# Kernel tuning notes

Measured on AMD Instinct MI355X. Metric: run time of the kernel, lower is better.

## Reference

```python
import jax, jax.numpy as jnp
import numpy as np

N, OBS_LEN, PRED_LEN = 8192, 20, 30
EMBED, HIDDEN, CNN_OUT = 64, 128, 2048


def setup_inputs() -> dict:
    key = jax.random.key(0)
    ks = jax.random.split(key, 13)
    s = 0.05
    return {
        "img_embedding": jax.random.normal(ks[0], (N, CNN_OUT), jnp.float32),
        "obs_pos": jax.random.normal(ks[1], (N, OBS_LEN, 2), jnp.float32),
        "obs_hist_size": jax.random.randint(ks[2], (N,), 0, 20, jnp.int64) if jax.config.jax_enable_x64 else jax.random.randint(ks[2], (N,), 0, 20, jnp.int32),
        "obs_pos_rel": jax.random.normal(ks[3], (N, OBS_LEN, 2), jnp.float32),
        "h0": jax.random.normal(ks[4], (1, HIDDEN), jnp.float32) * s,
        "W_ih": jax.random.normal(ks[5], (4 * HIDDEN, EMBED), jnp.float32) * s,
        "W_hh": jax.random.normal(ks[6], (4 * HIDDEN, HIDDEN), jnp.float32) * s,
        "b_ih": jax.random.normal(ks[7], (4 * HIDDEN,), jnp.float32) * s,
        "b_hh": jax.random.normal(ks[8], (4 * HIDDEN,), jnp.float32) * s,
        "embed_W": jax.random.normal(ks[9], (EMBED, 2), jnp.float32) * s,
        "embed_b": jax.random.normal(ks[10], (EMBED,), jnp.float32) * s,
        "pred_W": jax.random.normal(ks[11], (2, HIDDEN + CNN_OUT), jnp.float32) * s,
        "pred_b": jax.random.normal(ks[12], (2,), jnp.float32) * s,
    }


def reference(img_embedding, obs_pos, obs_hist_size, obs_pos_rel,
              h0, W_ih, W_hh, b_ih, b_hh, embed_W, embed_b, pred_W, pred_b):
    n, obs_len = obs_pos.shape[0], obs_pos.shape[1]

    def lstm_cell(x_emb, h, c):
        # torch gate order: i, f, g, o
        gates = x_emb @ W_ih.T + b_ih + h @ W_hh.T + b_hh  # [n, 4H]
        i, f, g, o = jnp.split(gates, 4, axis=-1)
        c2 = jax.nn.sigmoid(f) * c + jax.nn.sigmoid(i) * jnp.tanh(g)
        h2 = jax.nn.sigmoid(o) * jnp.tanh(c2)
        return h2, c2

    def embed(rel):
        return jax.nn.relu(rel @ embed_W.T + embed_b)

    # NOTE: original code initializes BOTH h and c from h0 (faithful to source).
    h = jnp.broadcast_to(h0, (n, h0.shape[1]))
    c = h

    # ---- observation phase: t = 1 .. obs_len-1, masked update ----
    def obs_step(carry, inp):
        h, c = carry
        rel_t, t = inp
        mask = (obs_hist_size > (obs_len - t))[:, None]  # [n, 1]
        h2, c2 = lstm_cell(embed(rel_t), h, c)
        h = jnp.where(mask, h2, h)
        c = jnp.where(mask, c2, c)
        return (h, c), None

    ts = jnp.arange(1, obs_len)
    rel_seq = jnp.swapaxes(obs_pos_rel[:, 1:, :], 0, 1)  # [obs_len-1, n, 2]
    (h, c), _ = jax.lax.scan(obs_step, (h, c), (rel_seq, ts))

    def pred_step(carry, _):
        h, c, pos = carry
        disp = jnp.concatenate([h, img_embedding], axis=1) @ pred_W.T + pred_b  # [n, 2]
        pos = pos + disp
        h, c = lstm_cell(embed(disp), h, c)
        return (h, c, pos), pos

    pos0 = obs_pos[:, -1, :]
    _, traj = jax.lax.scan(pred_step, (h, c, pos0), None, length=PRED_LEN)
    return jnp.swapaxes(traj, 0, 1)  # [n, pred_len, 2]
```

## Files before the change

### kernel.cpp

```cpp
#include <hip/hip_runtime.h>

#define MBLK 32

typedef __attribute__((ext_vector_type(8))) short bf16x8;
typedef __attribute__((ext_vector_type(4))) float f32x4;

__device__ __forceinline__ unsigned short f2bf(float x){
  unsigned int u = __float_as_uint(x);
  u = u + 0x7FFFu + ((u >> 16) & 1u);
  return (unsigned short)(u >> 16);
}
__device__ __forceinline__ float bf2f(unsigned short s){
  return __uint_as_float(((unsigned int)s) << 16);
}
__device__ __forceinline__ float sigm(float x){
  return __builtin_amdgcn_rcpf(1.0f + __expf(-x));
}
__device__ __forceinline__ float tanh_(float x){
  return 1.0f - 2.0f*__builtin_amdgcn_rcpf(__expf(2.0f*x) + 1.0f);
}

__global__ __launch_bounds__(512, 2) void traj_kernel(
    const float* __restrict__ img, const float* __restrict__ obs_pos,
    const int* __restrict__ hist, const float* __restrict__ rel,
    const float* __restrict__ h0, const float* __restrict__ W_ih,
    const float* __restrict__ W_hh, const float* __restrict__ b_ih,
    const float* __restrict__ b_hh, const float* __restrict__ eW,
    const float* __restrict__ eb, const float* __restrict__ pW,
    const float* __restrict__ pb, float* __restrict__ out)
{
  __shared__ unsigned short xh[2][MBLK*200];
  __shared__ float relL[MBLK*40];
  __shared__ float pwL[256];
  __shared__ float eW0[64], eW1[64], ebL[64];
  __shared__ float imgcL[MBLK*2];

  const int tid  = threadIdx.x;
  const int wv   = tid >> 6;
  const int lane = tid & 63;
  const int q    = lane >> 4;
  const int i    = lane & 15;
  const int j    = wv*16 + i;
  const int g0   = blockIdx.x * MBLK;

  for (int idx = tid; idx < MBLK*40; idx += 512) relL[idx] = rel[g0*40 + idx];
  if (tid < 256) pwL[tid] = pW[(tid >> 7)*2176 + (tid & 127)];
  if (tid < 64){ eW0[tid] = eW[tid*2]; eW1[tid] = eW[tid*2+1]; ebL[tid] = eb[tid]; }

  {
    int m = tid >> 4, i16 = tid & 15;
    const float* row = img + (size_t)(g0 + m)*2048 + i16*128;
    const float* p0  = pW + 128 + i16*128;
    const float* p1  = pW + 2176 + 128 + i16*128;
    float s0 = 0.f, s1 = 0.f;
    #pragma unroll
    for (int v = 0; v < 32; v++){
      float4 a  = ((const float4*)row)[v];
      float4 w0 = ((const float4*)p0)[v];
      float4 w1 = ((const float4*)p1)[v];
      s0 += a.x*w0.x + a.y*w0.y + a.z*w0.z + a.w*w0.w;
      s1 += a.x*w1.x + a.y*w1.y + a.z*w1.z + a.w*w1.w;
    }
    #pragma unroll
    for (int msk = 1; msk < 16; msk <<= 1){
      s0 += __shfl_xor(s0, msk);
      s1 += __shfl_xor(s1, msk);
    }
    if (i16 == 0){ imgcL[m*2] = s0; imgcL[m*2+1] = s1; }
  }

  float h0j = h0[j];
  float bias_s[4];
  #pragma unroll
  for (int nt = 0; nt < 4; nt++) bias_s[nt] = b_ih[nt*128 + j] + b_hh[nt*128 + j];

  int   hist_s[8];
  float c_s[8], h_s[8];
  #pragma unroll
  for (int mt = 0; mt < 2; mt++)
    #pragma unroll
    for (int r = 0; r < 4; r++){
      int m = mt*16 + q*4 + r;
      hist_s[mt*4+r] = hist[g0 + m];
      c_s[mt*4+r] = h0j; h_s[mt*4+r] = h0j;
      xh[0][m*200 + 64 + j] = f2bf(h0j);
    }

  bf16x8 Bf[4][6];
  #pragma unroll
  for (int nt = 0; nt < 4; nt++){
    int row = nt*128 + j;
    #pragma unroll
    for (int kt = 0; kt < 6; kt++){
      const float* src = (kt < 2) ? (W_ih + row*64  + kt*32      + q*8)
                                  : (W_hh + row*128 + (kt-2)*32  + q*8);
      float4 lo = ((const float4*)src)[0];
      float4 hi = ((const float4*)src)[1];
      bf16x8 tf;
      tf[0]=(short)f2bf(lo.x); tf[1]=(short)f2bf(lo.y); tf[2]=(short)f2bf(lo.z); tf[3]=(short)f2bf(lo.w);
      tf[4]=(short)f2bf(hi.x); tf[5]=(short)f2bf(hi.y); tf[6]=(short)f2bf(hi.z); tf[7]=(short)f2bf(hi.w);
      Bf[nt][kt] = tf;
    }
  }

  const int dm  = tid >> 4;
  const int i16 = tid & 15;
  float pos_r = 0.f;
  if (i16 < 2) pos_r = obs_pos[(size_t)(g0 + dm)*40 + 38 + i16];

  __syncthreads();

  const float imgc0 = imgcL[dm*2], imgc1 = imgcL[dm*2+1];
  const float pb0 = pb[0], pb1 = pb[1];

  {
    int e0 = i16 << 2;
    float r0 = relL[dm*40 + 2], r1 = relL[dm*40 + 3];
    float a0 = fmaxf(0.f, r0*eW0[e0+0] + r1*eW1[e0+0] + ebL[e0+0]);
    float a1 = fmaxf(0.f, r0*eW0[e0+1] + r1*eW1[e0+1] + ebL[e0+1]);
    float a2 = fmaxf(0.f, r0*eW0[e0+2] + r1*eW1[e0+2] + ebL[e0+2]);
    float a3 = fmaxf(0.f, r0*eW0[e0+3] + r1*eW1[e0+3] + ebL[e0+3]);
    unsigned int pk0 = (unsigned int)f2bf(a0) | ((unsigned int)f2bf(a1) << 16);
    unsigned int pk1 = (unsigned int)f2bf(a2) | ((unsigned int)f2bf(a3) << 16);
    *((uint2*)&xh[0][dm*200 + e0]) = make_uint2(pk0, pk1);
  }

  int b = 0;
  f32x4 acc[2][4];

  for (int step = 0; step < 49; step++){
    const bool obs = (step < 19);
    __syncthreads();

    if (!obs){
      bf16x8 hv = *((const bf16x8*)&xh[b][dm*200 + 64 + i16*8]);
      float s0 = 0.f, s1 = 0.f;
      #pragma unroll
      for (int u = 0; u < 8; u++){
        float hfv = bf2f((unsigned short)hv[u]);
        s0 += hfv * pwL[i16*8 + u];
        s1 += hfv * pwL[128 + i16*8 + u];
      }
      s0 += __shfl_xor(s0, 1); s1 += __shfl_xor(s1, 1);
      s0 += __shfl_xor(s0, 2); s1 += __shfl_xor(s1, 2);
      s0 += __shfl_xor(s0, 4); s1 += __shfl_xor(s1, 4);
      s0 += __shfl_xor(s0, 8); s1 += __shfl_xor(s1, 8);
      float d0 = s0 + imgc0 + pb0;
      float d1 = s1 + imgc1 + pb1;
      if (i16 < 2){
        pos_r += (i16 == 0) ? d0 : d1;
        out[(size_t)(g0 + dm)*60 + (size_t)(step - 19)*2 + i16] = pos_r;
      }
      int e0 = i16 << 2;
      float a0 = fmaxf(0.f, d0*eW0[e0+0] + d1*eW1[e0+0] + ebL[e0+0]);
      float a1 = fmaxf(0.f, d0*eW0[e0+1] + d1*eW1[e0+1] + ebL[e0+1]);
      float a2 = fmaxf(0.f, d0*eW0[e0+2] + d1*eW1[e0+2] + ebL[e0+2]);
      float a3 = fmaxf(0.f, d0*eW0[e0+3] + d1*eW1[e0+3] + ebL[e0+3]);
      unsigned int pk0 = (unsigned int)f2bf(a0) | ((unsigned int)f2bf(a1) << 16);
      unsigned int pk1 = (unsigned int)f2bf(a2) | ((unsigned int)f2bf(a3) << 16);
      *((uint2*)&xh[b][dm*200 + e0]) = make_uint2(pk0, pk1);
      __syncthreads();
    }

    #pragma unroll
    for (int mt = 0; mt < 2; mt++){
      bf16x8 A[6];
      int mrow = mt*16 + i;
      #pragma unroll
      for (int kt = 0; kt < 6; kt++)
        A[kt] = *((const bf16x8*)&xh[b][mrow*200 + kt*32 + q*8]);
      #pragma unroll
      for (int nt = 0; nt < 4; nt++)
        acc[mt][nt] = (f32x4){bias_s[nt], bias_s[nt], bias_s[nt], bias_s[nt]};
      #pragma unroll
      for (int kt = 0; kt < 6; kt++)
        #pragma unroll
        for (int nt = 0; nt < 4; nt++)
          acc[mt][nt] = __builtin_amdgcn_mfma_f32_16x16x32_bf16(A[kt], Bf[nt][kt], acc[mt][nt], 0, 0, 0);
    }

    if (obs && step < 18){
      int tt = step + 2;
      int e0 = i16 << 2;
      float r0 = relL[dm*40 + tt*2], r1 = relL[dm*40 + tt*2 + 1];
      float a0 = fmaxf(0.f, r0*eW0[e0+0] + r1*eW1[e0+0] + ebL[e0+0]);
      float a1 = fmaxf(0.f, r0*eW0[e0+1] + r1*eW1[e0+1] + ebL[e0+1]);
      float a2 = fmaxf(0.f, r0*eW0[e0+2] + r1*eW1[e0+2] + ebL[e0+2]);
      float a3 = fmaxf(0.f, r0*eW0[e0+3] + r1*eW1[e0+3] + ebL[e0+3]);
      unsigned int pk0 = (unsigned int)f2bf(a0) | ((unsigned int)f2bf(a1) << 16);
      unsigned int pk1 = (unsigned int)f2bf(a2) | ((unsigned int)f2bf(a3) << 16);
      *((uint2*)&xh[b^1][dm*200 + e0]) = make_uint2(pk0, pk1);
    }

    #pragma unroll
    for (int mt = 0; mt < 2; mt++)
      #pragma unroll
      for (int r = 0; r < 4; r++){
        int sl = mt*4 + r;
        float ig = acc[mt][0][r];
        float fg = acc[mt][1][r];
        float gg = acc[mt][2][r];
        float og = acc[mt][3][r];
        float c2 = sigm(fg)*c_s[sl] + sigm(ig)*tanh_(gg);
        float h2 = sigm(og)*tanh_(c2);
        if (obs){
          bool upd = hist_s[sl] > (19 - step);
          c2 = upd ? c2 : c_s[sl];
          h2 = upd ? h2 : h_s[sl];
        }
        c_s[sl] = c2; h_s[sl] = h2;
        int m = mt*16 + q*4 + r;
        xh[b^1][m*200 + 64 + j] = f2bf(h2);
      }

    b ^= 1;
  }
}

extern "C" void kernel_launch(void* const* d_in, const int* in_sizes, int n_in,
                              void* d_out, int out_size, void* d_ws, size_t ws_size,
                              hipStream_t stream){
  const float* img     = (const float*)d_in[0];
  const float* obs_pos = (const float*)d_in[1];
  const int*   hist    = (const int*)d_in[2];
  const float* rel     = (const float*)d_in[3];
  const float* h0      = (const float*)d_in[4];
  const float* W_ih    = (const float*)d_in[5];
  const float* W_hh    = (const float*)d_in[6];
  const float* b_ih    = (const float*)d_in[7];
  const float* b_hh    = (const float*)d_in[8];
  const float* eW      = (const float*)d_in[9];
  const float* eb      = (const float*)d_in[10];
  const float* pW      = (const float*)d_in[11];
  const float* pb      = (const float*)d_in[12];
  float* out = (float*)d_out;
  hipLaunchKernelGGL(traj_kernel, dim3(8192/MBLK), dim3(512), 0, stream,
                     img, obs_pos, hist, rel, h0, W_ih, W_hh, b_ih, b_hh,
                     eW, eb, pW, pb, out);
}
```

Baseline: 268.6 us.

## Split LSTM row tiles across 16 waves and stage output-gate weights in LDS

```diff
diff --git a/kernel.cpp b/kernel.cpp
--- a/kernel.cpp
+++ b/kernel.cpp
@@ -20,7 +20,7 @@
   return 1.0f - 2.0f*__builtin_amdgcn_rcpf(__expf(2.0f*x) + 1.0f);
 }
 
-__global__ __launch_bounds__(512, 2) void traj_kernel(
+__global__ __launch_bounds__(1024, 4) void traj_kernel(
     const float* __restrict__ img, const float* __restrict__ obs_pos,
     const int* __restrict__ hist, const float* __restrict__ rel,
     const float* __restrict__ h0, const float* __restrict__ W_ih,
@@ -30,6 +30,7 @@
     const float* __restrict__ pb, float* __restrict__ out)
 {
   __shared__ unsigned short xh[2][MBLK*200];
+  __shared__ unsigned short BoL[6*8*64*8];
   __shared__ float relL[MBLK*40];
   __shared__ float pwL[256];
   __shared__ float eW0[64], eW1[64], ebL[64];
@@ -40,21 +41,24 @@
   const int lane = tid & 63;
   const int q    = lane >> 4;
   const int i    = lane & 15;
-  const int j    = wv*16 + i;
+  const int w8   = wv & 7;
+  const int mtb  = (wv >> 3) << 4;
+  const int jw   = w8*16 + i;
   const int g0   = blockIdx.x * MBLK;
-
-  for (int idx = tid; idx < MBLK*40; idx += 512) relL[idx] = rel[g0*40 + idx];
+  const int dm   = tid >> 5;
+  const int i32  = tid & 31;
+
+  for (int idx = tid; idx < MBLK*40; idx += 1024) relL[idx] = rel[g0*40 + idx];
   if (tid < 256) pwL[tid] = pW[(tid >> 7)*2176 + (tid & 127)];
   if (tid < 64){ eW0[tid] = eW[tid*2]; eW1[tid] = eW[tid*2+1]; ebL[tid] = eb[tid]; }
 
   {
-    int m = tid >> 4, i16 = tid & 15;
-    const float* row = img + (size_t)(g0 + m)*2048 + i16*128;
-    const float* p0  = pW + 128 + i16*128;
-    const float* p1  = pW + 2176 + 128 + i16*128;
+    const float* row = img + (size_t)(g0 + dm)*2048 + i32*64;
+    const float* p0  = pW + 128 + i32*64;
+    const float* p1  = pW + 2176 + 128 + i32*64;
     float s0 = 0.f, s1 = 0.f;
     #pragma unroll
-    for (int v = 0; v < 32; v++){
+    for (int v = 0; v < 16; v++){
       float4 a  = ((const float4*)row)[v];
       float4 w0 = ((const float4*)p0)[v];
       float4 w1 = ((const float4*)p1)[v];
@@ -62,38 +66,37 @@
       s1 += a.x*w1.x + a.y*w1.y + a.z*w1.z + a.w*w1.w;
     }
     #pragma unroll
-    for (int msk = 1; msk < 16; msk <<= 1){
+    for (int msk = 1; msk < 32; msk <<= 1){
       s0 += __shfl_xor(s0, msk);
       s1 += __shfl_xor(s1, msk);
     }
-    if (i16 == 0){ imgcL[m*2] = s0; imgcL[m*2+1] = s1; }
-  }
-
-  float h0j = h0[j];
+    if (i32 == 0){ imgcL[dm*2] = s0; imgcL[dm*2+1] = s1; }
+  }
+
+  float h0j = h0[jw];
   float bias_s[4];
   #pragma unroll
-  for (int nt = 0; nt < 4; nt++) bias_s[nt] = b_ih[nt*128 + j] + b_hh[nt*128 + j];
-
-  int   hist_s[8];
-  float c_s[8], h_s[8];
+  for (int nt = 0; nt < 4; nt++) bias_s[nt] = b_ih[nt*128 + jw] + b_hh[nt*128 + jw];
+
+  unsigned int thrpack = 0;
+  float c_s[4], h_s[4];
   #pragma unroll
-  for (int mt = 0; mt < 2; mt++)
-    #pragma unroll
-    for (int r = 0; r < 4; r++){
-      int m = mt*16 + q*4 + r;
-      hist_s[mt*4+r] = hist[g0 + m];
-      c_s[mt*4+r] = h0j; h_s[mt*4+r] = h0j;
-      xh[0][m*200 + 64 + j] = f2bf(h0j);
-    }
-
-  bf16x8 Bf[4][6];
+  for (int r = 0; r < 4; r++){
+    int m = mtb + q*4 + r;
+    int hv = hist[g0 + m];
+    thrpack |= ((unsigned int)(20 - hv) & 255u) << (r*8);
+    c_s[r] = h0j; h_s[r] = h0j;
+    xh[0][m*200 + 64 + jw] = f2bf(h0j);
+  }
+
+  bf16x8 Bf[3][6];
   #pragma unroll
-  for (int nt = 0; nt < 4; nt++){
-    int row = nt*128 + j;
+  for (int nt = 0; nt < 3; nt++){
+    int row = nt*128 + jw;
     #pragma unroll
     for (int kt = 0; kt < 6; kt++){
-      const float* src = (kt < 2) ? (W_ih + row*64  + kt*32      + q*8)
-                                  : (W_hh + row*128 + (kt-2)*32  + q*8);
+      const float* src = (kt < 2) ? (W_ih + row*64  + kt*32     + q*8)
+                                  : (W_hh + row*128 + (kt-2)*32 + q*8);
       float4 lo = ((const float4*)src)[0];
       float4 hi = ((const float4*)src)[1];
       bf16x8 tf;
@@ -102,116 +105,112 @@
       Bf[nt][kt] = tf;
     }
   }
-
-  const int dm  = tid >> 4;
-  const int i16 = tid & 15;
+  if (wv < 8){
+    int row = 384 + jw;
+    #pragma unroll
+    for (int kt = 0; kt < 6; kt++){
+      const float* src = (kt < 2) ? (W_ih + row*64  + kt*32     + q*8)
+                                  : (W_hh + row*128 + (kt-2)*32 + q*8);
+      float4 lo = ((const float4*)src)[0];
+      float4 hi = ((const float4*)src)[1];
+      bf16x8 tf;
+      tf[0]=(short)f2bf(lo.x); tf[1]=(short)f2bf(lo.y); tf[2]=(short)f2bf(lo.z); tf[3]=(short)f2bf(lo.w);
+      tf[4]=(short)f2bf(hi.x); tf[5]=(short)f2bf(hi.y); tf[6]=(short)f2bf(hi.z); tf[7]=(short)f2bf(hi.w);
+      *((bf16x8*)&BoL[((kt*8 + w8)*64 + lane)*8]) = tf;
+    }
+  }
+
   float pos_r = 0.f;
-  if (i16 < 2) pos_r = obs_pos[(size_t)(g0 + dm)*40 + 38 + i16];
+  if (i32 < 2) pos_r = obs_pos[(size_t)(g0 + dm)*40 + 38 + i32];
 
   __syncthreads();
 
-  const float imgc0 = imgcL[dm*2], imgc1 = imgcL[dm*2+1];
-  const float pb0 = pb[0], pb1 = pb[1];
+  const float ipb0 = imgcL[dm*2]     + pb[0];
+  const float ipb1 = imgcL[dm*2 + 1] + pb[1];
 
   {
-    int e0 = i16 << 2;
+    int e2 = i32*2;
     float r0 = relL[dm*40 + 2], r1 = relL[dm*40 + 3];
-    float a0 = fmaxf(0.f, r0*eW0[e0+0] + r1*eW1[e0+0] + ebL[e0+0]);
-    float a1 = fmaxf(0.f, r0*eW0[e0+1] + r1*eW1[e0+1] + ebL[e0+1]);
-    float a2 = fmaxf(0.f, r0*eW0[e0+2] + r1*eW1[e0+2] + ebL[e0+2]);
-    float a3 = fmaxf(0.f, r0*eW0[e0+3] + r1*eW1[e0+3] + ebL[e0+3]);
-    unsigned int pk0 = (unsigned int)f2bf(a0) | ((unsigned int)f2bf(a1) << 16);
-    unsigned int pk1 = (unsigned int)f2bf(a2) | ((unsigned int)f2bf(a3) << 16);
-    *((uint2*)&xh[0][dm*200 + e0]) = make_uint2(pk0, pk1);
+    float a0 = fmaxf(0.f, r0*eW0[e2]   + r1*eW1[e2]   + ebL[e2]);
+    float a1 = fmaxf(0.f, r0*eW0[e2+1] + r1*eW1[e2+1] + ebL[e2+1]);
+    *((unsigned int*)&xh[0][dm*200 + e2]) =
+        (unsigned int)f2bf(a0) | ((unsigned int)f2bf(a1) << 16);
   }
 
   int b = 0;
-  f32x4 acc[2][4];
-
   for (int step = 0; step < 49; step++){
     const bool obs = (step < 19);
     __syncthreads();
 
     if (!obs){
-      bf16x8 hv = *((const bf16x8*)&xh[b][dm*200 + 64 + i16*8]);
+      const unsigned short* hp = &xh[b][dm*200 + 64 + i32*4];
       float s0 = 0.f, s1 = 0.f;
       #pragma unroll
-      for (int u = 0; u < 8; u++){
-        float hfv = bf2f((unsigned short)hv[u]);
-        s0 += hfv * pwL[i16*8 + u];
-        s1 += hfv * pwL[128 + i16*8 + u];
-      }
-      s0 += __shfl_xor(s0, 1); s1 += __shfl_xor(s1, 1);
-      s0 += __shfl_xor(s0, 2); s1 += __shfl_xor(s1, 2);
-      s0 += __shfl_xor(s0, 4); s1 += __shfl_xor(s1, 4);
-      s0 += __shfl_xor(s0, 8); s1 += __shfl_xor(s1, 8);
-      float d0 = s0 + imgc0 + pb0;
-      float d1 = s1 + imgc1 + pb1;
-      if (i16 < 2){
-        pos_r += (i16 == 0) ? d0 : d1;
-        out[(size_t)(g0 + dm)*60 + (size_t)(step - 19)*2 + i16] = pos_r;
-      }
-      int e0 = i16 << 2;
-      float a0 = fmaxf(0.f, d0*eW0[e0+0] + d1*eW1[e0+0] + ebL[e0+0]);
-      float a1 = fmaxf(0.f, d0*eW0[e0+1] + d1*eW1[e0+1] + ebL[e0+1]);
-      float a2 = fmaxf(0.f, d0*eW0[e0+2] + d1*eW1[e0+2] + ebL[e0+2]);
-      float a3 = fmaxf(0.f, d0*eW0[e0+3] + d1*eW1[e0+3] + ebL[e0+3]);
-      unsigned int pk0 = (unsigned int)f2bf(a0) | ((unsigned int)f2bf(a1) << 16);
-      unsigned int pk1 = (unsigned int)f2bf(a2) | ((unsigned int)f2bf(a3) << 16);
-      *((uint2*)&xh[b][dm*200 + e0]) = make_uint2(pk0, pk1);
+      for (int u = 0; u < 4; u++){
+        float hfv = bf2f(hp[u]);
+        s0 += hfv * pwL[i32*4 + u];
+        s1 += hfv * pwL[128 + i32*4 + u];
+      }
+      #pragma unroll
+      for (int msk = 1; msk < 32; msk <<= 1){
+        s0 += __shfl_xor(s0, msk);
+        s1 += __shfl_xor(s1, msk);
+      }
+      float d0 = s0 + ipb0;
+      float d1 = s1 + ipb1;
+      if (i32 < 2){
+        pos_r += (i32 == 0) ? d0 : d1;
+        out[(size_t)(g0 + dm)*60 + (size_t)(step - 19)*2 + i32] = pos_r;
+      }
+      int e2 = i32*2;
+      float a0 = fmaxf(0.f, d0*eW0[e2]   + d1*eW1[e2]   + ebL[e2]);
+      float a1 = fmaxf(0.f, d0*eW0[e2+1] + d1*eW1[e2+1] + ebL[e2+1]);
+      *((unsigned int*)&xh[b][dm*200 + e2]) =
+          (unsigned int)f2bf(a0) | ((unsigned int)f2bf(a1) << 16);
       __syncthreads();
     }
 
-    #pragma unroll
-    for (int mt = 0; mt < 2; mt++){
-      bf16x8 A[6];
-      int mrow = mt*16 + i;
-      #pragma unroll
-      for (int kt = 0; kt < 6; kt++)
-        A[kt] = *((const bf16x8*)&xh[b][mrow*200 + kt*32 + q*8]);
-      #pragma unroll
-      for (int nt = 0; nt < 4; nt++)
-        acc[mt][nt] = (f32x4){bias_s[nt], bias_s[nt], bias_s[nt], bias_s[nt]};
-      #pragma unroll
-      for (int kt = 0; kt < 6; kt++)
-        #pragma unroll
-        for (int nt = 0; nt < 4; nt++)
-          acc[mt][nt] = __builtin_amdgcn_mfma_f32_16x16x32_bf16(A[kt], Bf[nt][kt], acc[mt][nt], 0, 0, 0);
+    f32x4 acc[4];
+    #pragma unroll
+    for (int nt = 0; nt < 4; nt++)
+      acc[nt] = (f32x4){bias_s[nt], bias_s[nt], bias_s[nt], bias_s[nt]};
+    #pragma unroll
+    for (int kt = 0; kt < 6; kt++){
+      bf16x8 a  = *((const bf16x8*)&xh[b][(mtb + i)*200 + kt*32 + q*8]);
+      bf16x8 bo = *((const bf16x8*)&BoL[((kt*8 + w8)*64 + lane)*8]);
+      acc[0] = __builtin_amdgcn_mfma_f32_16x16x32_bf16(a, Bf[0][kt], acc[0], 0, 0, 0);
+      acc[1] = __builtin_amdgcn_mfma_f32_16x16x32_bf16(a, Bf[1][kt], acc[1], 0, 0, 0);
+      acc[2] = __builtin_amdgcn_mfma_f32_16x16x32_bf16(a, Bf[2][kt], acc[2], 0, 0, 0);
+      acc[3] = __builtin_amdgcn_mfma_f32_16x16x32_bf16(a, bo,        acc[3], 0, 0, 0);
     }
 
     if (obs && step < 18){
       int tt = step + 2;
-      int e0 = i16 << 2;
+      int e2 = i32*2;
       float r0 = relL[dm*40 + tt*2], r1 = relL[dm*40 + tt*2 + 1];
-      float a0 = fmaxf(0.f, r0*eW0[e0+0] + r1*eW1[e0+0] + ebL[e0+0]);
-      float a1 = fmaxf(0.f, r0*eW0[e0+1] + r1*eW1[e0+1] + ebL[e0+1]);
-      float a2 = fmaxf(0.f, r0*eW0[e0+2] + r1*eW1[e0+2] + ebL[e0+2]);
-      float a3 = fmaxf(0.f, r0*eW0[e0+3] + r1*eW1[e0+3] + ebL[e0+3]);
-      unsigned int pk0 = (unsigned int)f2bf(a0) | ((unsigned int)f2bf(a1) << 16);
-      unsigned int pk1 = (unsigned int)f2bf(a2) | ((unsigned int)f2bf(a3) << 16);
-      *((uint2*)&xh[b^1][dm*200 + e0]) = make_uint2(pk0, pk1);
-    }
-
-    #pragma unroll
-    for (int mt = 0; mt < 2; mt++)
-      #pragma unroll
-      for (int r = 0; r < 4; r++){
-        int sl = mt*4 + r;
-        float ig = acc[mt][0][r];
-        float fg = acc[mt][1][r];
-        float gg = acc[mt][2][r];
-        float og = acc[mt][3][r];
-        float c2 = sigm(fg)*c_s[sl] + sigm(ig)*tanh_(gg);
-        float h2 = sigm(og)*tanh_(c2);
-        if (obs){
-          bool upd = hist_s[sl] > (19 - step);
-          c2 = upd ? c2 : c_s[sl];
-          h2 = upd ? h2 : h_s[sl];
-        }
-        c_s[sl] = c2; h_s[sl] = h2;
-        int m = mt*16 + q*4 + r;
-        xh[b^1][m*200 + 64 + j] = f2bf(h2);
-      }
+      float a0 = fmaxf(0.f, r0*eW0[e2]   + r1*eW1[e2]   + ebL[e2]);
+      float a1 = fmaxf(0.f, r0*eW0[e2+1] + r1*eW1[e2+1] + ebL[e2+1]);
+      *((unsigned int*)&xh[b^1][dm*200 + e2]) =
+          (unsigned int)f2bf(a0) | ((unsigned int)f2bf(a1) << 16);
+    }
+
+    #pragma unroll
+    for (int r = 0; r < 4; r++){
+      float ig = acc[0][r];
+      float fg = acc[1][r];
+      float gg = acc[2][r];
+      float og = acc[3][r];
+      float c2 = sigm(fg)*c_s[r] + sigm(ig)*tanh_(gg);
+      float h2 = sigm(og)*tanh_(c2);
+      if (obs){
+        bool upd = (int)((thrpack >> (r*8)) & 255u) <= step;
+        c2 = upd ? c2 : c_s[r];
+        h2 = upd ? h2 : h_s[r];
+      }
+      c_s[r] = c2; h_s[r] = h2;
+      int m = mtb + q*4 + r;
+      xh[b^1][m*200 + 64 + jw] = f2bf(h2);
+    }
 
     b ^= 1;
   }
@@ -234,7 +233,7 @@
   const float* pW      = (const float*)d_in[11];
   const float* pb      = (const float*)d_in[12];
   float* out = (float*)d_out;
-  hipLaunchKernelGGL(traj_kernel, dim3(8192/MBLK), dim3(512), 0, stream,
+  hipLaunchKernelGGL(traj_kernel, dim3(8192/MBLK), dim3(1024), 0, stream,
                      img, obs_pos, hist, rel, h0, W_ih, W_hh, b_ih, b_hh,
                      eW, eb, pW, pb, out);
 }
```

After: 480.6 us. +79.0%, slower.
